# Optimization experiments

Measured on AMD Instinct MI355X. Metric: run time of the kernel, lower is better.

## Reference

```python
import jax, jax.numpy as jnp
import numpy as np

B, NQ, NK, D_EQUI, D_INV, D_MSG, D_FF, D_OUT = 2, 768, 768, 256, 256, 32, 128, 64


def setup_inputs() -> dict:
    key = jax.random.key(0)
    ks = jax.random.split(key, 14)
    s = 0.05  # weight init scale
    inp = {
        'q_equi': jax.random.normal(ks[0], (B, NQ, 3, D_EQUI), dtype=jnp.float32),
        'q_inv': jax.random.normal(ks[1], (B, NQ, D_INV), dtype=jnp.float32),
        'k_equi': jax.random.normal(ks[2], (B, NK, 3, D_EQUI), dtype=jnp.float32),
        'k_inv': jax.random.normal(ks[3], (B, NK, D_INV), dtype=jnp.float32),
        # projection params (stored [in, out]; torch Linear is [out, in])
        'Wqi': jax.random.normal(ks[4], (D_INV, D_MSG), dtype=jnp.float32) * s,
        'bqi': jnp.zeros((D_MSG,), jnp.float32),
        'Wki': jax.random.normal(ks[5], (D_INV, D_MSG), dtype=jnp.float32) * s,
        'bki': jnp.zeros((D_MSG,), jnp.float32),
        'Wqe': jax.random.normal(ks[6], (D_EQUI, D_MSG), dtype=jnp.float32) * s,
        'bqe': jnp.zeros((D_MSG,), jnp.float32),
        'Wke': jax.random.normal(ks[7], (D_EQUI, D_MSG), dtype=jnp.float32) * s,
        'bke': jnp.zeros((D_MSG,), jnp.float32),
        # message MLP: in_feats = 4*d_message (q_inv, k_inv, dotprods, dists)
        'W1': jax.random.normal(ks[8], (4 * D_MSG, D_FF), dtype=jnp.float32) * s,
        'b1': jnp.zeros((D_FF,), jnp.float32),
        'W2': jax.random.normal(ks[9], (D_FF, D_OUT), dtype=jnp.float32) * s,
        'b2': jnp.zeros((D_OUT,), jnp.float32),
    }
    return inp


def reference(q_equi, q_inv, k_equi, k_inv, Wqi, bqi, Wki, bki, Wqe, bqe, Wke, bke, W1, b1, W2, b2):
    b, nq = q_inv.shape[0], q_inv.shape[1]
    nk = k_inv.shape[1]
    # invariant projections -> [B, N, m]
    qi = q_inv @ Wqi + bqi
    ki = k_inv @ Wki + bki
    # equivariant projections -> [B, N, 3, m]
    qe = q_equi @ Wqe + bqe
    ke = k_equi @ Wke + bke
    # pairwise dot products over the 3D coordinate axis -> [B, Nq, Nk, m]
    dotprods = jnp.einsum('bqcm,bkcm->bqkm', qe, ke)
    # pairwise vector distances -> [B, Nq, Nk, m]
    vec = qe[:, :, None, :, :] - ke[:, None, :, :, :]  # [B, Nq, Nk, 3, m]
    dists = jnp.sqrt(jnp.sum(vec * vec, axis=3))
    feats = jnp.concatenate([
        jnp.broadcast_to(qi[:, :, None, :], (b, nq, nk, qi.shape[-1])),
        jnp.broadcast_to(ki[:, None, :, :], (b, nq, nk, ki.shape[-1])),
        dotprods,
        dists,
    ], axis=-1)  # [B, Nq, Nk, 4m]
    h = jax.nn.silu(feats @ W1 + b1)
    return h @ W2 + b2  # [B, Nq, Nk, d_out]
```

## Files before the change

kernel.cpp:

```cpp
#include <hip/hip_runtime.h>
#include <cstdint>

#define B_    2
#define NQ_   768
#define NK_   768
#define DE_   256
#define DI_   256
#define DM_   32
#define FF_   128
#define DO_   64

typedef float    f32x4 __attribute__((ext_vector_type(4)));
typedef _Float16 half8 __attribute__((ext_vector_type(8)));

__global__ __launch_bounds__(128) void node_pre_all(
    const float* __restrict__ q_inv, const float* __restrict__ q_equi,
    const float* __restrict__ k_inv, const float* __restrict__ k_equi,
    const float* __restrict__ Wqi, const float* __restrict__ bqi,
    const float* __restrict__ Wki, const float* __restrict__ bki,
    const float* __restrict__ Wqe, const float* __restrict__ bqe,
    const float* __restrict__ Wke, const float* __restrict__ bke,
    const float* __restrict__ W1,  const float* __restrict__ b1,
    const float* __restrict__ W2,
    float* __restrict__ qe, float* __restrict__ qq, float* __restrict__ Aq,
    float* __restrict__ ke, float* __restrict__ kk, float* __restrict__ Bk,
    _Float16* __restrict__ pk)
{
  const int side = blockIdx.y;
  const int t = threadIdx.x;

  if (blockIdx.x == B_*NQ_) {
    if (side == 0) {
      for (int i = t; i < 8192; i += 128) {
        const int j = i & 7, ln = (i>>3)&63, s = (i>>9)&1, nt = i>>10;
        const int row = 64 + s*32 + (ln>>4)*8 + j, col = nt*16 + (ln&15);
        pk[i] = (_Float16)W1[row*FF_ + col];
      }
    } else {
      for (int i = t; i < 8192; i += 128) {
        const int j = i & 7, ln = (i>>3)&63, s = (i>>9)&3, nt = i>>11;
        const int row = s*32 + (ln>>4)*8 + j, col = nt*16 + (ln&15);
        pk[8192 + i] = (_Float16)W2[row*DO_ + col];
      }
    }
    return;
  }

  const float* inv  = side ? k_inv  : q_inv;
  const float* equi = side ? k_equi : q_equi;
  const float* Wi   = side ? Wki : Wqi;
  const float* bi   = side ? bki : bqi;
  const float* We   = side ? Wke : Wqe;
  const float* be   = side ? bke : bqe;
  const int w1RowOff = side ? 32 : 0;
  const int addB1    = side ? 0 : 1;
  float* e_out  = side ? ke : qe;
  float* sq_out = side ? kk : qq;
  float* ab_out = side ? Bk : Aq;

  __shared__ float inv_s[DI_];
  __shared__ float equi_s[3*DE_];
  __shared__ float qi_s[DM_];
  __shared__ float e_s[96];
  const int node = blockIdx.x;
  const float* invp = inv  + (size_t)node*DI_;
  const float* eqp  = equi + (size_t)node*3*DE_;
  for (int i = t; i < DI_;   i += 128) inv_s[i]  = invp[i];
  for (int i = t; i < 3*DE_; i += 128) equi_s[i] = eqp[i];
  __syncthreads();
  if (t < 96) {
    const int c = t >> 5, m = t & 31;
    const float* eq = equi_s + c*DE_;
    float a0 = be[m], a1 = 0.f, a2 = 0.f, a3 = 0.f;
    #pragma unroll 4
    for (int d = 0; d < DE_; d += 4) {
      a0 = fmaf(eq[d+0], We[(d+0)*DM_+m], a0);
      a1 = fmaf(eq[d+1], We[(d+1)*DM_+m], a1);
      a2 = fmaf(eq[d+2], We[(d+2)*DM_+m], a2);
      a3 = fmaf(eq[d+3], We[(d+3)*DM_+m], a3);
    }
    const float acc = (a0+a1)+(a2+a3);
    e_s[t] = acc;
    e_out[(size_t)node*96 + t] = acc;
  } else {
    const int m = t & 31;
    float a0 = bi[m], a1 = 0.f, a2 = 0.f, a3 = 0.f;
    #pragma unroll 4
    for (int d = 0; d < DI_; d += 4) {
      a0 = fmaf(inv_s[d+0], Wi[(d+0)*DM_+m], a0);
      a1 = fmaf(inv_s[d+1], Wi[(d+1)*DM_+m], a1);
      a2 = fmaf(inv_s[d+2], Wi[(d+2)*DM_+m], a2);
      a3 = fmaf(inv_s[d+3], Wi[(d+3)*DM_+m], a3);
    }
    qi_s[m] = (a0+a1)+(a2+a3);
  }
  __syncthreads();
  if (t < 32) {
    const float v0 = e_s[t], v1 = e_s[32+t], v2 = e_s[64+t];
    sq_out[(size_t)node*32 + t] = v0*v0 + v1*v1 + v2*v2;
  }
  float acc = addB1 ? b1[t] : 0.f;
  #pragma unroll
  for (int m = 0; m < DM_; ++m)
    acc = fmaf(qi_s[m], W1[(w1RowOff + m)*FF_ + t], acc);
  ab_out[(size_t)node*FF_ + t] = acc;
}

__global__ __launch_bounds__(256, 2) void pair_main(
    const float* __restrict__ qe_g, const float* __restrict__ ke_g,
    const float* __restrict__ qq_g, const float* __restrict__ kk_g,
    const float* __restrict__ Aq_g, const float* __restrict__ Bk_g,
    const _Float16* __restrict__ pk, const float* __restrict__ b2,
    float* __restrict__ out)
{
  __shared__ __align__(16) float qe_s[8*100];
  __shared__ __align__(16) float ke_s[16*100];
  __shared__ __align__(16) float qq_s[8*36];
  __shared__ __align__(16) float kk_s[16*36];
  __shared__ __align__(16) float A_s[8*132];
  __shared__ __align__(16) float B_s[16*132];
  __shared__ __align__(16) unsigned char hs_raw[128*136*2];
  _Float16* h_s = (_Float16*)hs_raw;
  float*    o_s = (float*)hs_raw;

  const int tid = threadIdx.x;
  const int b  = blockIdx.z;
  const int q0 = blockIdx.y * 8;
  const int k0 = blockIdx.x * 16;

  { const float* p = qe_g + ((size_t)b*NQ_ + q0)*96;
    for (int i = tid; i < 8*96;  i += 256) qe_s[(i/96)*100 + (i%96)] = p[i]; }
  { const float* p = ke_g + ((size_t)b*NK_ + k0)*96;
    for (int i = tid; i < 16*96; i += 256) ke_s[(i/96)*100 + (i%96)] = p[i]; }
  { const float* p = qq_g + ((size_t)b*NQ_ + q0)*32;
    for (int i = tid; i < 8*32;  i += 256) qq_s[(i>>5)*36 + (i&31)] = p[i]; }
  { const float* p = kk_g + ((size_t)b*NK_ + k0)*32;
    for (int i = tid; i < 16*32; i += 256) kk_s[(i>>5)*36 + (i&31)] = p[i]; }
  { const float* p = Aq_g + ((size_t)b*NQ_ + q0)*128;
    for (int i = tid; i < 8*128; i += 256) A_s[(i>>7)*132 + (i&127)] = p[i]; }
  { const float* p = Bk_g + ((size_t)b*NK_ + k0)*128;
    for (int i = tid; i < 16*128; i += 256) B_s[(i>>7)*132 + (i&127)] = p[i]; }
  __syncthreads();

  const int lane = tid & 63;
  const int w    = tid >> 6;
  const int n15  = lane & 15;
  const int quad = lane >> 4;
  const int mq   = quad * 8;

  const half8* pk1 = (const half8*)pk;
  half8 B1[8][2];
  #pragma unroll
  for (int nt = 0; nt < 8; ++nt)
    #pragma unroll
    for (int s = 0; s < 2; ++s)
      B1[nt][s] = pk1[((nt*2 + s)<<6) + lane];

  f32x4 acc1[2][8];
  #pragma unroll
  for (int t = 0; t < 2; ++t)
    #pragma unroll
    for (int nt = 0; nt < 8; ++nt)
      acc1[t][nt] = (f32x4){0.f, 0.f, 0.f, 0.f};

  f32x4 keF[6], kkF[2];
  #pragma unroll
  for (int c = 0; c < 3; ++c) {
    keF[c*2+0] = *(const f32x4*)&ke_s[n15*100 + c*32 + mq];
    keF[c*2+1] = *(const f32x4*)&ke_s[n15*100 + c*32 + mq + 4];
  }
  kkF[0] = *(const f32x4*)&kk_s[n15*36 + mq];
  kkF[1] = *(const f32x4*)&kk_s[n15*36 + mq + 4];

  #pragma unroll
  for (int t = 0; t < 2; ++t) {
    const int qL = 2*w + t;
    f32x4 qeF[6], qqF[2];
    #pragma unroll
    for (int c = 0; c < 3; ++c) {
      qeF[c*2+0] = *(const f32x4*)&qe_s[qL*100 + c*32 + mq];
      qeF[c*2+1] = *(const f32x4*)&qe_s[qL*100 + c*32 + mq + 4];
    }
    qqF[0] = *(const f32x4*)&qq_s[qL*36 + mq];
    qqF[1] = *(const f32x4*)&qq_s[qL*36 + mq + 4];

    half8 A0, A1;
    float dots[8];
    #pragma unroll
    for (int j = 0; j < 8; ++j) {
      const int h = j >> 2, e = j & 3;
      float d = qeF[0+h][e] * keF[0+h][e];
      d = fmaf(qeF[2+h][e], keF[2+h][e], d);
      d = fmaf(qeF[4+h][e], keF[4+h][e], d);
      dots[j] = d;
      A0[j] = (_Float16)d;
    }
    #pragma unroll
    for (int j = 0; j < 8; ++j) {
      const int h = j >> 2, e = j & 3;
      float v = qqF[h][e] + kkF[h][e] - 2.f*dots[j];
      v = fmaxf(v, 0.f);
      A1[j] = (_Float16)__builtin_sqrtf(v);
    }
    #pragma unroll
    for (int nt = 0; nt < 8; ++nt) {
      acc1[t][nt] = __builtin_amdgcn_mfma_f32_16x16x32_f16(A0, B1[nt][0], acc1[t][nt], 0, 0, 0);
      acc1[t][nt] = __builtin_amdgcn_mfma_f32_16x16x32_f16(A1, B1[nt][1], acc1[t][nt], 0, 0, 0);
    }
  }

  #pragma unroll
  for (int nt = 0; nt < 8; ++nt) {
    const int f = (nt<<4) + n15;
    float Bv[4];
    #pragma unroll
    for (int r = 0; r < 4; ++r) Bv[r] = B_s[(quad*4+r)*132 + f];
    #pragma unroll
    for (int t = 0; t < 2; ++t) {
      const int qL = 2*w + t;
      const float Av = A_s[qL*132 + f];
      #pragma unroll
      for (int r = 0; r < 4; ++r) {
        const float x = acc1[t][nt][r] + Av + Bv[r];
        const float e = __builtin_amdgcn_exp2f(-1.44269504f * x);
        h_s[(qL*16 + quad*4 + r)*136 + f] = (_Float16)(x * __builtin_amdgcn_rcpf(1.f + e));
      }
    }
  }

  const half8* pk2 = (const half8*)(pk + 8192);
  half8 B2[4][4];
  #pragma unroll
  for (int nt = 0; nt < 4; ++nt)
    #pragma unroll
    for (int s = 0; s < 4; ++s)
      B2[nt][s] = pk2[((nt*4 + s)<<6) + lane];

  f32x4 acc2[2][4];
  #pragma unroll
  for (int t = 0; t < 2; ++t)
    #pragma unroll
    for (int nt = 0; nt < 4; ++nt)
      acc2[t][nt] = (f32x4){0.f,0.f,0.f,0.f};

  #pragma unroll
  for (int t = 0; t < 2; ++t) {
    const int qL = 2*w + t;
    #pragma unroll
    for (int s = 0; s < 4; ++s) {
      const half8 A2 = *(const half8*)&h_s[(qL*16 + n15)*136 + s*32 + mq];
      #pragma unroll
      for (int nt = 0; nt < 4; ++nt)
        acc2[t][nt] = __builtin_amdgcn_mfma_f32_16x16x32_f16(A2, B2[nt][s], acc2[t][nt], 0, 0, 0);
    }
  }

  float bias[4];
  #pragma unroll
  for (int nt = 0; nt < 4; ++nt) bias[nt] = b2[(nt<<4) + n15];
  #pragma unroll
  for (int nt = 0; nt < 4; ++nt) {
    const int o = (nt<<4) + n15;
    #pragma unroll
    for (int t = 0; t < 2; ++t) {
      const int qL = 2*w + t;
      #pragma unroll
      for (int r = 0; r < 4; ++r)
        o_s[(qL*16 + quad*4 + r)*68 + o] = acc2[t][nt][r] + bias[nt];
    }
  }
  __syncthreads();

  const size_t outBase = (((size_t)b*NQ_ + q0)*NK_ + k0)*DO_;
  #pragma unroll
  for (int c = 0; c < 8; ++c) {
    const int idx  = c*256 + tid;
    const int pair = idx >> 4;
    const int o4   = (idx & 15) << 2;
    const int qL   = pair >> 4;
    const int kL   = pair & 15;
    const f32x4 v = *(const f32x4*)&o_s[pair*68 + o4];
    *(f32x4*)&out[outBase + ((size_t)qL*NK_ + kL)*DO_ + o4] = v;
  }
}

extern "C" void kernel_launch(void* const* d_in, const int* in_sizes, int n_in,
                              void* d_out, int out_size, void* d_ws, size_t ws_size,
                              hipStream_t stream) {
  const float* q_equi = (const float*)d_in[0];
  const float* q_inv  = (const float*)d_in[1];
  const float* k_equi = (const float*)d_in[2];
  const float* k_inv  = (const float*)d_in[3];
  const float* Wqi = (const float*)d_in[4];
  const float* bqi = (const float*)d_in[5];
  const float* Wki = (const float*)d_in[6];
  const float* bki = (const float*)d_in[7];
  const float* Wqe = (const float*)d_in[8];
  const float* bqe = (const float*)d_in[9];
  const float* Wke = (const float*)d_in[10];
  const float* bke = (const float*)d_in[11];
  const float* W1  = (const float*)d_in[12];
  const float* b1  = (const float*)d_in[13];
  const float* W2  = (const float*)d_in[14];
  const float* b2  = (const float*)d_in[15];

  float* ws = (float*)d_ws;
  float* qe = ws;
  float* ke = qe + (size_t)B_*NQ_*96;
  float* qq = ke + (size_t)B_*NK_*96;
  float* kk = qq + (size_t)B_*NQ_*32;
  float* Aq = kk + (size_t)B_*NK_*32;
  float* Bk = Aq + (size_t)B_*NQ_*128;
  _Float16* pk = (_Float16*)(Bk + (size_t)B_*NK_*128);

  dim3 ngrid(B_*NQ_ + 1, 2);
  node_pre_all<<<ngrid, 128, 0, stream>>>(
      q_inv, q_equi, k_inv, k_equi, Wqi, bqi, Wki, bki, Wqe, bqe, Wke, bke,
      W1, b1, W2, qe, qq, Aq, ke, kk, Bk, pk);

  dim3 grid(NK_/16, NQ_/8, B_);
  pair_main<<<grid, 256, 0, stream>>>(qe, ke, qq, kk, Aq, Bk, pk, b2, (float*)d_out);
}
```

Baseline: 464.5 us.

## Restructure pair kernel to transpose MFMAs, shrink LDS, and batch node preprocessing

The node preprocessing kernel now handles four nodes per 256-thread block and stages the projection weights in LDS so they are reused across nodes. The pair kernel swaps the MFMA operand order to get a transposed layout, computes the first MLP layer one query at a time, and streams W1/W2 fragments from global instead of holding them in registers. The large shared h/o buffer becomes a small per-wave h tile, and output is written straight from accumulators without an LDS round-trip or final barrier. Occupancy rises to 4 blocks per SM via launch bounds, at the cost of repeated fragment loads and less coalesced output stores.

```diff
diff --git a/kernel.cpp b/kernel.cpp
--- a/kernel.cpp
+++ b/kernel.cpp
@@ -9,11 +9,13 @@
 #define DM_   32
 #define FF_   128
 #define DO_   64
-
-typedef float    f32x4 __attribute__((ext_vector_type(4)));
-typedef _Float16 half8 __attribute__((ext_vector_type(8)));
-
-__global__ __launch_bounds__(128) void node_pre_all(
+#define NB_   4
+
+typedef float    f32x4  __attribute__((ext_vector_type(4)));
+typedef _Float16 half8  __attribute__((ext_vector_type(8)));
+typedef _Float16 half2v __attribute__((ext_vector_type(2)));
+
+__global__ __launch_bounds__(256) void node_pre_all(
     const float* __restrict__ q_inv, const float* __restrict__ q_equi,
     const float* __restrict__ k_inv, const float* __restrict__ k_equi,
     const float* __restrict__ Wqi, const float* __restrict__ bqi,
@@ -29,15 +31,15 @@
   const int side = blockIdx.y;
   const int t = threadIdx.x;
 
-  if (blockIdx.x == B_*NQ_) {
+  if (blockIdx.x == (B_*NQ_)/NB_) {
     if (side == 0) {
-      for (int i = t; i < 8192; i += 128) {
+      for (int i = t; i < 8192; i += 256) {
         const int j = i & 7, ln = (i>>3)&63, s = (i>>9)&1, nt = i>>10;
         const int row = 64 + s*32 + (ln>>4)*8 + j, col = nt*16 + (ln&15);
         pk[i] = (_Float16)W1[row*FF_ + col];
       }
     } else {
-      for (int i = t; i < 8192; i += 128) {
+      for (int i = t; i < 8192; i += 256) {
         const int j = i & 7, ln = (i>>3)&63, s = (i>>9)&3, nt = i>>11;
         const int row = s*32 + (ln>>4)*8 + j, col = nt*16 + (ln&15);
         pk[8192 + i] = (_Float16)W2[row*DO_ + col];
@@ -58,55 +60,77 @@
   float* sq_out = side ? kk : qq;
   float* ab_out = side ? Bk : Aq;
 
-  __shared__ float inv_s[DI_];
-  __shared__ float equi_s[3*DE_];
-  __shared__ float qi_s[DM_];
-  __shared__ float e_s[96];
-  const int node = blockIdx.x;
-  const float* invp = inv  + (size_t)node*DI_;
-  const float* eqp  = equi + (size_t)node*3*DE_;
-  for (int i = t; i < DI_;   i += 128) inv_s[i]  = invp[i];
-  for (int i = t; i < 3*DE_; i += 128) equi_s[i] = eqp[i];
-  __syncthreads();
-  if (t < 96) {
-    const int c = t >> 5, m = t & 31;
-    const float* eq = equi_s + c*DE_;
-    float a0 = be[m], a1 = 0.f, a2 = 0.f, a3 = 0.f;
-    #pragma unroll 4
-    for (int d = 0; d < DE_; d += 4) {
-      a0 = fmaf(eq[d+0], We[(d+0)*DM_+m], a0);
-      a1 = fmaf(eq[d+1], We[(d+1)*DM_+m], a1);
-      a2 = fmaf(eq[d+2], We[(d+2)*DM_+m], a2);
-      a3 = fmaf(eq[d+3], We[(d+3)*DM_+m], a3);
-    }
-    const float acc = (a0+a1)+(a2+a3);
-    e_s[t] = acc;
-    e_out[(size_t)node*96 + t] = acc;
-  } else {
-    const int m = t & 31;
-    float a0 = bi[m], a1 = 0.f, a2 = 0.f, a3 = 0.f;
-    #pragma unroll 4
-    for (int d = 0; d < DI_; d += 4) {
-      a0 = fmaf(inv_s[d+0], Wi[(d+0)*DM_+m], a0);
-      a1 = fmaf(inv_s[d+1], Wi[(d+1)*DM_+m], a1);
-      a2 = fmaf(inv_s[d+2], Wi[(d+2)*DM_+m], a2);
-      a3 = fmaf(inv_s[d+3], Wi[(d+3)*DM_+m], a3);
-    }
-    qi_s[m] = (a0+a1)+(a2+a3);
-  }
-  __syncthreads();
-  if (t < 32) {
-    const float v0 = e_s[t], v1 = e_s[32+t], v2 = e_s[64+t];
-    sq_out[(size_t)node*32 + t] = v0*v0 + v1*v1 + v2*v2;
-  }
-  float acc = addB1 ? b1[t] : 0.f;
-  #pragma unroll
-  for (int m = 0; m < DM_; ++m)
-    acc = fmaf(qi_s[m], W1[(w1RowOff + m)*FF_ + t], acc);
-  ab_out[(size_t)node*FF_ + t] = acc;
+  __shared__ __align__(16) float W_s[DE_*DM_];
+  __shared__ __align__(16) float eq_s[NB_*3*DE_];
+  __shared__ __align__(16) float inv_s[NB_*DI_];
+  __shared__ float e_s[NB_*96];
+  __shared__ float qi_s[NB_*DM_];
+
+  const int node0 = blockIdx.x * NB_;
+
+  { const f32x4* g = (const f32x4*)(equi + (size_t)node0*3*DE_);
+    f32x4* d = (f32x4*)eq_s;
+    #pragma unroll
+    for (int i = 0; i < 3; ++i) d[t + 256*i] = g[t + 256*i]; }
+  { const f32x4* g = (const f32x4*)(inv + (size_t)node0*DI_);
+    ((f32x4*)inv_s)[t] = g[t]; }
+  { const f32x4* g = (const f32x4*)We;
+    f32x4* d = (f32x4*)W_s;
+    #pragma unroll
+    for (int i = 0; i < 8; ++i) d[t + 256*i] = g[t + 256*i]; }
+  __syncthreads();
+
+  auto dotW = [&](const float* __restrict__ x, const int m) -> float {
+    float a0 = 0.f, a1 = 0.f, a2 = 0.f, a3 = 0.f;
+    #pragma unroll 16
+    for (int d = 0; d < 256; d += 4) {
+      a0 = fmaf(x[d+0], W_s[(d+0)*DM_ + m], a0);
+      a1 = fmaf(x[d+1], W_s[(d+1)*DM_ + m], a1);
+      a2 = fmaf(x[d+2], W_s[(d+2)*DM_ + m], a2);
+      a3 = fmaf(x[d+3], W_s[(d+3)*DM_ + m], a3);
+    }
+    return (a0+a1)+(a2+a3);
+  };
+
+  { const int node = t>>6, c = (t>>5)&1, m = t&31;
+    const float v = be[m] + dotW(eq_s + node*3*DE_ + c*DE_, m);
+    e_s[node*96 + c*32 + m] = v;
+    e_out[(size_t)(node0+node)*96 + c*32 + m] = v; }
+  if (t < 128) {
+    const int node = t>>5, m = t&31;
+    const float v = be[m] + dotW(eq_s + node*3*DE_ + 2*DE_, m);
+    e_s[node*96 + 64 + m] = v;
+    e_out[(size_t)(node0+node)*96 + 64 + m] = v; }
+  __syncthreads();
+
+  { const f32x4* g = (const f32x4*)Wi;
+    f32x4* d = (f32x4*)W_s;
+    #pragma unroll
+    for (int i = 0; i < 8; ++i) d[t + 256*i] = g[t + 256*i]; }
+  if (t < NB_*32) {
+    const int node = t>>5, m = t&31;
+    const float v0 = e_s[node*96+m], v1 = e_s[node*96+32+m], v2 = e_s[node*96+64+m];
+    sq_out[(size_t)(node0+node)*32 + m] = v0*v0 + v1*v1 + v2*v2; }
+  __syncthreads();
+
+  if (t < NB_*32) {
+    const int node = t>>5, m = t&31;
+    qi_s[node*32 + m] = bi[m] + dotW(inv_s + node*DI_, m); }
+  __syncthreads();
+
+  #pragma unroll
+  for (int oo = 0; oo < 2; ++oo) {
+    const int o = t + oo*256;
+    const int node = o>>7, f = o&127;
+    float acc = addB1 ? b1[f] : 0.f;
+    #pragma unroll
+    for (int m = 0; m < DM_; ++m)
+      acc = fmaf(qi_s[node*32 + m], W1[(w1RowOff+m)*FF_ + f], acc);
+    ab_out[(size_t)(node0+node)*FF_ + f] = acc;
+  }
 }
 
-__global__ __launch_bounds__(256, 2) void pair_main(
+__global__ __launch_bounds__(256, 4) void pair_main(
     const float* __restrict__ qe_g, const float* __restrict__ ke_g,
     const float* __restrict__ qq_g, const float* __restrict__ kk_g,
     const float* __restrict__ Aq_g, const float* __restrict__ Bk_g,
@@ -119,27 +143,25 @@
   __shared__ __align__(16) float kk_s[16*36];
   __shared__ __align__(16) float A_s[8*132];
   __shared__ __align__(16) float B_s[16*132];
-  __shared__ __align__(16) unsigned char hs_raw[128*136*2];
-  _Float16* h_s = (_Float16*)hs_raw;
-  float*    o_s = (float*)hs_raw;
+  __shared__ __align__(16) _Float16 h_t[4][16*72];
 
   const int tid = threadIdx.x;
   const int b  = blockIdx.z;
   const int q0 = blockIdx.y * 8;
   const int k0 = blockIdx.x * 16;
 
-  { const float* p = qe_g + ((size_t)b*NQ_ + q0)*96;
-    for (int i = tid; i < 8*96;  i += 256) qe_s[(i/96)*100 + (i%96)] = p[i]; }
-  { const float* p = ke_g + ((size_t)b*NK_ + k0)*96;
-    for (int i = tid; i < 16*96; i += 256) ke_s[(i/96)*100 + (i%96)] = p[i]; }
-  { const float* p = qq_g + ((size_t)b*NQ_ + q0)*32;
-    for (int i = tid; i < 8*32;  i += 256) qq_s[(i>>5)*36 + (i&31)] = p[i]; }
-  { const float* p = kk_g + ((size_t)b*NK_ + k0)*32;
-    for (int i = tid; i < 16*32; i += 256) kk_s[(i>>5)*36 + (i&31)] = p[i]; }
-  { const float* p = Aq_g + ((size_t)b*NQ_ + q0)*128;
-    for (int i = tid; i < 8*128; i += 256) A_s[(i>>7)*132 + (i&127)] = p[i]; }
-  { const float* p = Bk_g + ((size_t)b*NK_ + k0)*128;
-    for (int i = tid; i < 16*128; i += 256) B_s[(i>>7)*132 + (i&127)] = p[i]; }
+  { const f32x4* p = (const f32x4*)(qe_g + ((size_t)b*NQ_ + q0)*96);
+    if (tid < 192) ((f32x4*)qe_s)[(tid/24)*25 + tid%24] = p[tid]; }
+  { const f32x4* p = (const f32x4*)(ke_g + ((size_t)b*NK_ + k0)*96);
+    for (int i = tid; i < 384; i += 256) ((f32x4*)ke_s)[(i/24)*25 + i%24] = p[i]; }
+  { const f32x4* p = (const f32x4*)(qq_g + ((size_t)b*NQ_ + q0)*32);
+    if (tid < 64) ((f32x4*)qq_s)[(tid>>3)*9 + (tid&7)] = p[tid]; }
+  { const f32x4* p = (const f32x4*)(kk_g + ((size_t)b*NK_ + k0)*32);
+    if (tid < 128) ((f32x4*)kk_s)[(tid>>3)*9 + (tid&7)] = p[tid]; }
+  { const f32x4* p = (const f32x4*)(Aq_g + ((size_t)b*NQ_ + q0)*128);
+    ((f32x4*)A_s)[(tid>>5)*33 + (tid&31)] = p[tid]; }
+  { const f32x4* p = (const f32x4*)(Bk_g + ((size_t)b*NK_ + k0)*128);
+    for (int i = tid; i < 512; i += 256) ((f32x4*)B_s)[(i>>5)*33 + (i&31)] = p[i]; }
   __syncthreads();
 
   const int lane = tid & 63;
@@ -149,38 +171,31 @@
   const int mq   = quad * 8;
 
   const half8* pk1 = (const half8*)pk;
-  half8 B1[8][2];
-  #pragma unroll
-  for (int nt = 0; nt < 8; ++nt)
-    #pragma unroll
-    for (int s = 0; s < 2; ++s)
-      B1[nt][s] = pk1[((nt*2 + s)<<6) + lane];
-
-  f32x4 acc1[2][8];
+  const half8* pk2 = (const half8*)(pk + 8192);
+  _Float16* hrow = &h_t[w][n15*72];
+
+  half8 H[2][4];
+  f32x4 acc2[2][4];
   #pragma unroll
   for (int t = 0; t < 2; ++t)
     #pragma unroll
-    for (int nt = 0; nt < 8; ++nt)
-      acc1[t][nt] = (f32x4){0.f, 0.f, 0.f, 0.f};
-
-  f32x4 keF[6], kkF[2];
-  #pragma unroll
-  for (int c = 0; c < 3; ++c) {
-    keF[c*2+0] = *(const f32x4*)&ke_s[n15*100 + c*32 + mq];
-    keF[c*2+1] = *(const f32x4*)&ke_s[n15*100 + c*32 + mq + 4];
-  }
-  kkF[0] = *(const f32x4*)&kk_s[n15*36 + mq];
-  kkF[1] = *(const f32x4*)&kk_s[n15*36 + mq + 4];
+    for (int nt = 0; nt < 4; ++nt)
+      acc2[t][nt] = (f32x4){0.f,0.f,0.f,0.f};
 
   #pragma unroll
   for (int t = 0; t < 2; ++t) {
     const int qL = 2*w + t;
-    f32x4 qeF[6], qqF[2];
+
+    f32x4 keF[6], kkF[2], qeF[6], qqF[2];
     #pragma unroll
     for (int c = 0; c < 3; ++c) {
+      keF[c*2+0] = *(const f32x4*)&ke_s[n15*100 + c*32 + mq];
+      keF[c*2+1] = *(const f32x4*)&ke_s[n15*100 + c*32 + mq + 4];
       qeF[c*2+0] = *(const f32x4*)&qe_s[qL*100 + c*32 + mq];
       qeF[c*2+1] = *(const f32x4*)&qe_s[qL*100 + c*32 + mq + 4];
     }
+    kkF[0] = *(const f32x4*)&kk_s[n15*36 + mq];
+    kkF[1] = *(const f32x4*)&kk_s[n15*36 + mq + 4];
     qqF[0] = *(const f32x4*)&qq_s[qL*36 + mq];
     qqF[1] = *(const f32x4*)&qq_s[qL*36 + mq + 4];
 
@@ -202,85 +217,74 @@
       v = fmaxf(v, 0.f);
       A1[j] = (_Float16)__builtin_sqrtf(v);
     }
-    #pragma unroll
-    for (int nt = 0; nt < 8; ++nt) {
-      acc1[t][nt] = __builtin_amdgcn_mfma_f32_16x16x32_f16(A0, B1[nt][0], acc1[t][nt], 0, 0, 0);
-      acc1[t][nt] = __builtin_amdgcn_mfma_f32_16x16x32_f16(A1, B1[nt][1], acc1[t][nt], 0, 0, 0);
-    }
-  }
-
-  #pragma unroll
-  for (int nt = 0; nt < 8; ++nt) {
-    const int f = (nt<<4) + n15;
-    float Bv[4];
-    #pragma unroll
-    for (int r = 0; r < 4; ++r) Bv[r] = B_s[(quad*4+r)*132 + f];
-    #pragma unroll
-    for (int t = 0; t < 2; ++t) {
-      const int qL = 2*w + t;
-      const float Av = A_s[qL*132 + f];
-      #pragma unroll
-      for (int r = 0; r < 4; ++r) {
-        const float x = acc1[t][nt][r] + Av + Bv[r];
-        const float e = __builtin_amdgcn_exp2f(-1.44269504f * x);
-        h_s[(qL*16 + quad*4 + r)*136 + f] = (_Float16)(x * __builtin_amdgcn_rcpf(1.f + e));
+
+    f32x4 acc1[8];
+    #pragma unroll
+    for (int nt = 0; nt < 8; ++nt) acc1[nt] = (f32x4){0.f,0.f,0.f,0.f};
+    {
+      half8 B1s[8];
+      #pragma unroll
+      for (int nt = 0; nt < 8; ++nt) B1s[nt] = pk1[((nt*2 + 0)<<6) + lane];
+      #pragma unroll
+      for (int nt = 0; nt < 8; ++nt)
+        acc1[nt] = __builtin_amdgcn_mfma_f32_16x16x32_f16(B1s[nt], A0, acc1[nt], 0, 0, 0);
+      #pragma unroll
+      for (int nt = 0; nt < 8; ++nt) B1s[nt] = pk1[((nt*2 + 1)<<6) + lane];
+      #pragma unroll
+      for (int nt = 0; nt < 8; ++nt)
+        acc1[nt] = __builtin_amdgcn_mfma_f32_16x16x32_f16(B1s[nt], A1, acc1[nt], 0, 0, 0);
+    }
+
+    #pragma unroll
+    for (int ch = 0; ch < 2; ++ch) {
+      #pragma unroll
+      for (int ntl = 0; ntl < 4; ++ntl) {
+        const int nt = ch*4 + ntl;
+        const f32x4 Af = *(const f32x4*)&A_s[qL*132 + nt*16 + quad*4];
+        const f32x4 Bf = *(const f32x4*)&B_s[n15*132 + nt*16 + quad*4];
+        _Float16 hv[4];
+        #pragma unroll
+        for (int r = 0; r < 4; ++r) {
+          const float x = acc1[nt][r] + Af[r] + Bf[r];
+          const float e = __builtin_amdgcn_exp2f(-1.44269504f * x);
+          hv[r] = (_Float16)(x * __builtin_amdgcn_rcpf(1.f + e));
+        }
+        half2v p0; p0[0] = hv[0]; p0[1] = hv[1];
+        half2v p1; p1[0] = hv[2]; p1[1] = hv[3];
+        *(half2v*)&hrow[ntl*16 + quad*4 + 0] = p0;
+        *(half2v*)&hrow[ntl*16 + quad*4 + 2] = p1;
       }
-    }
-  }
-
-  const half8* pk2 = (const half8*)(pk + 8192);
-  half8 B2[4][4];
-  #pragma unroll
-  for (int nt = 0; nt < 4; ++nt)
-    #pragma unroll
-    for (int s = 0; s < 4; ++s)
-      B2[nt][s] = pk2[((nt*4 + s)<<6) + lane];
-
-  f32x4 acc2[2][4];
-  #pragma unroll
-  for (int t = 0; t < 2; ++t)
-    #pragma unroll
-    for (int nt = 0; nt < 4; ++nt)
-      acc2[t][nt] = (f32x4){0.f,0.f,0.f,0.f};
-
+      #pragma unroll
+      for (int sl = 0; sl < 2; ++sl)
+        H[t][ch*2 + sl] = *(const half8*)&hrow[sl*32 + mq];
+    }
+  }
+
+  #pragma unroll
+  for (int s = 0; s < 4; ++s) {
+    half8 B2s[4];
+    #pragma unroll
+    for (int nt = 0; nt < 4; ++nt) B2s[nt] = pk2[((nt*4 + s)<<6) + lane];
+    #pragma unroll
+    for (int t = 0; t < 2; ++t)
+      #pragma unroll
+      for (int nt = 0; nt < 4; ++nt)
+        acc2[t][nt] = __builtin_amdgcn_mfma_f32_16x16x32_f16(B2s[nt], H[t][s], acc2[t][nt], 0, 0, 0);
+  }
+
+  f32x4 bias[4];
+  #pragma unroll
+  for (int nt = 0; nt < 4; ++nt) bias[nt] = *(const f32x4*)&b2[nt*16 + quad*4];
+  const size_t outBase = (((size_t)b*NQ_ + q0)*NK_ + k0)*DO_;
   #pragma unroll
   for (int t = 0; t < 2; ++t) {
     const int qL = 2*w + t;
-    #pragma unroll
-    for (int s = 0; s < 4; ++s) {
-      const half8 A2 = *(const half8*)&h_s[(qL*16 + n15)*136 + s*32 + mq];
-      #pragma unroll
-      for (int nt = 0; nt < 4; ++nt)
-        acc2[t][nt] = __builtin_amdgcn_mfma_f32_16x16x32_f16(A2, B2[nt][s], acc2[t][nt], 0, 0, 0);
-    }
-  }
-
-  float bias[4];
-  #pragma unroll
-  for (int nt = 0; nt < 4; ++nt) bias[nt] = b2[(nt<<4) + n15];
-  #pragma unroll
-  for (int nt = 0; nt < 4; ++nt) {
-    const int o = (nt<<4) + n15;
-    #pragma unroll
-    for (int t = 0; t < 2; ++t) {
-      const int qL = 2*w + t;
-      #pragma unroll
-      for (int r = 0; r < 4; ++r)
-        o_s[(qL*16 + quad*4 + r)*68 + o] = acc2[t][nt][r] + bias[nt];
-    }
-  }
-  __syncthreads();
-
-  const size_t outBase = (((size_t)b*NQ_ + q0)*NK_ + k0)*DO_;
-  #pragma unroll
-  for (int c = 0; c < 8; ++c) {
-    const int idx  = c*256 + tid;
-    const int pair = idx >> 4;
-    const int o4   = (idx & 15) << 2;
-    const int qL   = pair >> 4;
-    const int kL   = pair & 15;
-    const f32x4 v = *(const f32x4*)&o_s[pair*68 + o4];
-    *(f32x4*)&out[outBase + ((size_t)qL*NK_ + kL)*DO_ + o4] = v;
+    float* orow = out + outBase + ((size_t)qL*NK_ + n15)*DO_;
+    #pragma unroll
+    for (int nt = 0; nt < 4; ++nt) {
+      const f32x4 v = acc2[t][nt] + bias[nt];
+      *(f32x4*)&orow[nt*16 + quad*4] = v;
+    }
   }
 }
 
@@ -313,8 +317,8 @@
   float* Bk = Aq + (size_t)B_*NQ_*128;
   _Float16* pk = (_Float16*)(Bk + (size_t)B_*NK_*128);
 
-  dim3 ngrid(B_*NQ_ + 1, 2);
-  node_pre_all<<<ngrid, 128, 0, stream>>>(
+  dim3 ngrid(B_*NQ_/NB_ + 1, 2);
+  node_pre_all<<<ngrid, 256, 0, stream>>>(
       q_inv, q_equi, k_inv, k_equi, Wqi, bqi, Wki, bki, Wqe, bqe, Wke, bke,
       W1, b1, W2, qe, qq, Aq, ke, kk, Bk, pk);
 
```

Result: faster. 413.2 us (-11.0%).
